# Optimization experiments

Measured on AMD Instinct MI355X. Metric: run time of the kernel, lower is better.

Reference implementation:

```python
import jax, jax.numpy as jnp
import numpy as np

NEG_SLOPE = 0.2  # LeakyReLU(0.2)


def setup_inputs() -> dict:
    key = jax.random.key(0)
    k0, k1, kw, kb = jax.random.split(key, 4)
    B, N, M, D, H = 1, 1024, 1024, 256, 128
    z0 = jax.random.normal(k0, (B, N, D), dtype=jnp.float32)
    z1 = jax.random.normal(k1, (B, M, D), dtype=jnp.float32)
    # Conv2d(D, H, 1) weight (H, D, 1, 1) squeezed to (H, D); bias (H,)
    W = jax.random.normal(kw, (H, D), dtype=jnp.float32) * (1.0 / np.sqrt(D))
    bias = jax.random.normal(kb, (H,), dtype=jnp.float32) * 0.01
    return {"z0": z0, "z1": z1, "W": W, "bias": bias}


def reference(z0, z1, W, bias):
    # torch: z_mul[b,d,n,m] = z0[b,n,d] * z1[b,m,d]; c = conv1x1(z_mul); LeakyReLU
    # Fused: 1x1 conv over channel D is a contraction -> single einsum, no (b,D,N,M) intermediate.
    c = jnp.einsum('bnd,bmd,hd->bhnm', z0, z1, W) + bias[None, :, None, None]
    return jnp.where(c >= 0, c, NEG_SLOPE * c)
```

## Files before the change

### kernel.cpp

```cpp
#include <hip/hip_runtime.h>
#include <cstdint>

#define AS1 __attribute__((address_space(1)))
#define AS3 __attribute__((address_space(3)))

typedef __bf16 v8bf __attribute__((ext_vector_type(8)));
typedef float  v4f  __attribute__((ext_vector_type(4)));

__device__ __forceinline__ uint32_t f2u(float f) {
    union { float f; uint32_t u; } v; v.f = f; return v.u;
}
__device__ __forceinline__ uint16_t f2bf_rne(float f) {
    uint32_t u = f2u(f);
    return (uint16_t)((u + 0x7FFFu + ((u >> 16) & 1u)) >> 16);
}
__device__ __forceinline__ uint32_t pack2(float a, float b) {
    return (uint32_t)f2bf_rne(a) | ((uint32_t)f2bf_rne(b) << 16);
}
__device__ __forceinline__ void async16(const void* g, void* l) {
    __builtin_amdgcn_global_load_lds((AS1 const void*)g, (AS3 void*)l, 16, 0, 0);
}

__global__ __launch_bounds__(256)
void prep_kernel(const float* __restrict__ z0, const float* __restrict__ z1,
                 const float* __restrict__ W,
                 uint16_t* __restrict__ Aall, uint16_t* __restrict__ Bbf)
{
    const int b = blockIdx.x;
    if (b < 16384) {
        const size_t e0 = ((size_t)b * 256 + threadIdx.x) * 8;
        const int h  = (int)(e0 >> 18);
        const int nd = (int)(e0 & 0x3FFFFu);
        const int d0 = (int)(e0 & 255u);
        float4 za = *(const float4*)(z0 + nd);
        float4 zb = *(const float4*)(z0 + nd + 4);
        float4 wa = *(const float4*)(W + h * 256 + d0);
        float4 wb = *(const float4*)(W + h * 256 + d0 + 4);
        uint4 r;
        r.x = pack2(za.x * wa.x, za.y * wa.y);
        r.y = pack2(za.z * wa.z, za.w * wa.w);
        r.z = pack2(zb.x * wb.x, zb.y * wb.y);
        r.w = pack2(zb.z * wb.z, zb.w * wb.w);
        *(uint4*)(Aall + e0) = r;
    } else {
        const size_t e0 = ((size_t)(b - 16384) * 256 + threadIdx.x) * 8;
        float4 za = *(const float4*)(z1 + e0);
        float4 zb = *(const float4*)(z1 + e0 + 4);
        uint4 r;
        r.x = pack2(za.x, za.y);
        r.y = pack2(za.z, za.w);
        r.z = pack2(zb.x, zb.y);
        r.w = pack2(zb.z, zb.w);
        *(uint4*)(Bbf + e0) = r;
    }
}

__global__ __launch_bounds__(256)
void gemm_kernel(const uint16_t* __restrict__ Aall, const uint16_t* __restrict__ Bbf,
                 const float* __restrict__ bias, float* __restrict__ out)
{
    __shared__ __align__(16) uint16_t aT[2][128 * 64];
    __shared__ __align__(16) uint16_t bT[2][128 * 64];

    const int t = threadIdx.x, wave = t >> 6, lane = t & 63;

    const int wg   = blockIdx.x;
    const int work = ((wg & 7) << 10) | (wg >> 3);
    const int h    = work >> 6;
    const int n0   = ((work >> 3) & 7) << 7;
    const int m0   = (work & 7) << 7;

    const uint16_t* Ab = Aall + ((size_t)h << 18) + ((size_t)n0 << 8);
    const uint16_t* Bb = Bbf + ((size_t)m0 << 8);

    const int srow = lane >> 3;
    const int slot = lane & 7;
    const int swz8 = (slot ^ srow) << 3;

    v4f acc[4][4];
#pragma unroll
    for (int r = 0; r < 4; ++r)
#pragma unroll
        for (int c = 0; c < 4; ++c) acc[r][c] = (v4f){0.f, 0.f, 0.f, 0.f};

    const int mbw = (wave & 1) * 64;
    const int nb  = (wave >> 1) * 64;
    const int fr  = lane & 15;
    const int q   = lane >> 4;
    const int sx  = fr & 7;

#pragma unroll
    for (int j = 0; j < 4; ++j) {
        const int row = wave * 32 + j * 8;
        async16(Ab + (size_t)(row + srow) * 256 + swz8, &aT[0][row * 64]);
        async16(Bb + (size_t)(row + srow) * 256 + swz8, &bT[0][row * 64]);
    }
    __syncthreads();

#pragma unroll
    for (int ks = 0; ks < 4; ++ks) {
        const int cur = ks & 1, nxt = cur ^ 1;
        if (ks < 3) {
            const int kel = (ks + 1) * 64 + swz8;
#pragma unroll
            for (int j = 0; j < 4; ++j) {
                const int row = wave * 32 + j * 8;
                async16(Ab + (size_t)(row + srow) * 256 + kel, &aT[nxt][row * 64]);
                async16(Bb + (size_t)(row + srow) * 256 + kel, &bT[nxt][row * 64]);
            }
        }
#pragma unroll
        for (int ksl = 0; ksl < 2; ++ksl) {
            const int ko = ((((ksl << 2) | q) ^ sx) << 3);
            v8bf am[4], bn[4];
#pragma unroll
            for (int r = 0; r < 4; ++r)
                am[r] = *(const v8bf*)&bT[cur][(mbw + r * 16 + fr) * 64 + ko];
#pragma unroll
            for (int c = 0; c < 4; ++c)
                bn[c] = *(const v8bf*)&aT[cur][(nb + c * 16 + fr) * 64 + ko];
#pragma unroll
            for (int r = 0; r < 4; ++r)
#pragma unroll
                for (int c = 0; c < 4; ++c)
                    acc[r][c] = __builtin_amdgcn_mfma_f32_16x16x32_bf16(am[r], bn[c], acc[r][c], 0, 0, 0);
        }
        __syncthreads();
    }

    const float bsf = bias[h];
    float* outB = out + ((size_t)h << 20) + ((size_t)n0 << 10) + m0;
    const int mq = (lane >> 4) * 4;
#pragma unroll
    for (int r = 0; r < 4; ++r) {
#pragma unroll
        for (int c = 0; c < 4; ++c) {
            const int n = nb + c * 16 + fr;
            const int m = mbw + r * 16 + mq;
            float4 o;
            float v0 = acc[r][c][0] + bsf; o.x = (v0 >= 0.f) ? v0 : 0.2f * v0;
            float v1 = acc[r][c][1] + bsf; o.y = (v1 >= 0.f) ? v1 : 0.2f * v1;
            float v2 = acc[r][c][2] + bsf; o.z = (v2 >= 0.f) ? v2 : 0.2f * v2;
            float v3 = acc[r][c][3] + bsf; o.w = (v3 >= 0.f) ? v3 : 0.2f * v3;
            *(float4*)(outB + ((size_t)n << 10) + m) = o;
        }
    }
}

__global__ __launch_bounds__(256)
void gemm_fb(const float* __restrict__ z0, const float* __restrict__ z1,
             const float* __restrict__ W, const float* __restrict__ bias,
             float* __restrict__ out)
{
    __shared__ __align__(16) uint16_t aT[128 * 32];
    __shared__ __align__(16) uint16_t bT[128 * 32];
    const int t = threadIdx.x, wave = t >> 6, lane = t & 63;
    const int h = blockIdx.z, n0 = blockIdx.y * 128, m0 = blockIdx.x * 128;
    const float* Ab = z0 + (size_t)n0 * 256;
    const float* Bb = z1 + (size_t)m0 * 256;
    const int rowA = t >> 2, col8 = (t & 3) * 8;

    v4f acc[4][4];
#pragma unroll
    for (int r = 0; r < 4; ++r)
#pragma unroll
        for (int c = 0; c < 4; ++c) acc[r][c] = (v4f){0.f, 0.f, 0.f, 0.f};

    const int mbw = (wave & 1) * 64, nb = (wave >> 1) * 64;
    const int fr = lane & 15, kq = (lane >> 4) * 8;

    for (int ks = 0; ks < 8; ++ks) {
        const int k0 = ks * 32;
        float4 wa = *(const float4*)(W + h * 256 + k0 + col8);
        float4 wb = *(const float4*)(W + h * 256 + k0 + col8 + 4);
#pragma unroll
        for (int i = 0; i < 2; ++i) {
            const int row = i * 64 + rowA;
            float4 za = *(const float4*)(Ab + (size_t)row * 256 + k0 + col8);
            float4 zb = *(const float4*)(Ab + (size_t)row * 256 + k0 + col8 + 4);
            uint4 r;
            r.x = pack2(za.x * wa.x, za.y * wa.y);
            r.y = pack2(za.z * wa.z, za.w * wa.w);
            r.z = pack2(zb.x * wb.x, zb.y * wb.y);
            r.w = pack2(zb.z * wb.z, zb.w * wb.w);
            *(uint4*)&aT[(i * 256 + t) * 8] = r;
            float4 ba = *(const float4*)(Bb + (size_t)row * 256 + k0 + col8);
            float4 bb = *(const float4*)(Bb + (size_t)row * 256 + k0 + col8 + 4);
            uint4 s;
            s.x = pack2(ba.x, ba.y);
            s.y = pack2(ba.z, ba.w);
            s.z = pack2(bb.x, bb.y);
            s.w = pack2(bb.z, bb.w);
            *(uint4*)&bT[(i * 256 + t) * 8] = s;
        }
        __syncthreads();

        v8bf am[4], bn[4];
#pragma unroll
        for (int r = 0; r < 4; ++r)
            am[r] = *(const v8bf*)&bT[(mbw + r * 16 + fr) * 32 + kq];
#pragma unroll
        for (int c = 0; c < 4; ++c)
            bn[c] = *(const v8bf*)&aT[(nb + c * 16 + fr) * 32 + kq];
#pragma unroll
        for (int r = 0; r < 4; ++r)
#pragma unroll
            for (int c = 0; c < 4; ++c)
                acc[r][c] = __builtin_amdgcn_mfma_f32_16x16x32_bf16(am[r], bn[c], acc[r][c], 0, 0, 0);
        __syncthreads();
    }

    const float bsf = bias[h];
    float* outB = out + ((size_t)h << 20) + ((size_t)n0 << 10) + m0;
    const int mq = (lane >> 4) * 4;
#pragma unroll
    for (int r = 0; r < 4; ++r) {
#pragma unroll
        for (int c = 0; c < 4; ++c) {
            const int n = nb + c * 16 + fr;
            const int m = mbw + r * 16 + mq;
            float4 o;
            float v0 = acc[r][c][0] + bsf; o.x = (v0 >= 0.f) ? v0 : 0.2f * v0;
            float v1 = acc[r][c][1] + bsf; o.y = (v1 >= 0.f) ? v1 : 0.2f * v1;
            float v2 = acc[r][c][2] + bsf; o.z = (v2 >= 0.f) ? v2 : 0.2f * v2;
            float v3 = acc[r][c][3] + bsf; o.w = (v3 >= 0.f) ? v3 : 0.2f * v3;
            *(float4*)(outB + ((size_t)n << 10) + m) = o;
        }
    }
}

extern "C" void kernel_launch(void* const* d_in, const int* in_sizes, int n_in,
                              void* d_out, int out_size, void* d_ws, size_t ws_size,
                              hipStream_t stream) {
    (void)in_sizes; (void)n_in; (void)out_size;
    const float* z0   = (const float*)d_in[0];
    const float* z1   = (const float*)d_in[1];
    const float* Wm   = (const float*)d_in[2];
    const float* bias = (const float*)d_in[3];
    float* out = (float*)d_out;

    const size_t aall_bytes = (size_t)128 * 1024 * 256 * 2;
    const size_t need = aall_bytes + (size_t)1024 * 256 * 2;
    if (ws_size >= need) {
        uint16_t* Aall = (uint16_t*)d_ws;
        uint16_t* Bbf  = (uint16_t*)((char*)d_ws + aall_bytes);
        prep_kernel<<<16512, 256, 0, stream>>>(z0, z1, Wm, Aall, Bbf);
        gemm_kernel<<<8192, 256, 0, stream>>>(Aall, Bbf, bias, out);
    } else {
        dim3 grid(8, 8, 128), block(256);
        gemm_fb<<<grid, block, 0, stream>>>(z0, z1, Wm, bias, out);
    }
}
```

Measured before the change: 666.5 us.

## Fuse W-scaling and bf16 conversion into GEMM, drop prep kernel and workspace

Replaces the two-kernel path (prep writing a per-head W-scaled bf16 copy of z0, then a GEMM reading it) with a single kernel. Each thread loads a row slice of fp32 z0 or z1 into registers, scales by W for the A side, converts to bf16 and stores swizzled into double-buffered LDS. Register prefetch of the next k-slice overlaps the MFMAs. This removes the large intermediate write/read and a launch, at the cost of more registers and per-block conversion ALU work.

```diff
diff --git a/kernel.cpp b/kernel.cpp
--- a/kernel.cpp
+++ b/kernel.cpp
@@ -1,63 +1,13 @@
 #include <hip/hip_runtime.h>
 #include <cstdint>
-
-#define AS1 __attribute__((address_space(1)))
-#define AS3 __attribute__((address_space(3)))
 
 typedef __bf16 v8bf __attribute__((ext_vector_type(8)));
 typedef float  v4f  __attribute__((ext_vector_type(4)));
 
-__device__ __forceinline__ uint32_t f2u(float f) {
-    union { float f; uint32_t u; } v; v.f = f; return v.u;
-}
-__device__ __forceinline__ uint16_t f2bf_rne(float f) {
-    uint32_t u = f2u(f);
-    return (uint16_t)((u + 0x7FFFu + ((u >> 16) & 1u)) >> 16);
-}
-__device__ __forceinline__ uint32_t pack2(float a, float b) {
-    return (uint32_t)f2bf_rne(a) | ((uint32_t)f2bf_rne(b) << 16);
-}
-__device__ __forceinline__ void async16(const void* g, void* l) {
-    __builtin_amdgcn_global_load_lds((AS1 const void*)g, (AS3 void*)l, 16, 0, 0);
-}
-
 __global__ __launch_bounds__(256)
-void prep_kernel(const float* __restrict__ z0, const float* __restrict__ z1,
-                 const float* __restrict__ W,
-                 uint16_t* __restrict__ Aall, uint16_t* __restrict__ Bbf)
-{
-    const int b = blockIdx.x;
-    if (b < 16384) {
-        const size_t e0 = ((size_t)b * 256 + threadIdx.x) * 8;
-        const int h  = (int)(e0 >> 18);
-        const int nd = (int)(e0 & 0x3FFFFu);
-        const int d0 = (int)(e0 & 255u);
-        float4 za = *(const float4*)(z0 + nd);
-        float4 zb = *(const float4*)(z0 + nd + 4);
-        float4 wa = *(const float4*)(W + h * 256 + d0);
-        float4 wb = *(const float4*)(W + h * 256 + d0 + 4);
-        uint4 r;
-        r.x = pack2(za.x * wa.x, za.y * wa.y);
-        r.y = pack2(za.z * wa.z, za.w * wa.w);
-        r.z = pack2(zb.x * wb.x, zb.y * wb.y);
-        r.w = pack2(zb.z * wb.z, zb.w * wb.w);
-        *(uint4*)(Aall + e0) = r;
-    } else {
-        const size_t e0 = ((size_t)(b - 16384) * 256 + threadIdx.x) * 8;
-        float4 za = *(const float4*)(z1 + e0);
-        float4 zb = *(const float4*)(z1 + e0 + 4);
-        uint4 r;
-        r.x = pack2(za.x, za.y);
-        r.y = pack2(za.z, za.w);
-        r.z = pack2(zb.x, zb.y);
-        r.w = pack2(zb.z, zb.w);
-        *(uint4*)(Bbf + e0) = r;
-    }
-}
-
-__global__ __launch_bounds__(256)
-void gemm_kernel(const uint16_t* __restrict__ Aall, const uint16_t* __restrict__ Bbf,
-                 const float* __restrict__ bias, float* __restrict__ out)
+void fused_gemm(const float* __restrict__ z0, const float* __restrict__ z1,
+                const float* __restrict__ W, const float* __restrict__ bias,
+                float* __restrict__ out)
 {
     __shared__ __align__(16) uint16_t aT[2][128 * 64];
     __shared__ __align__(16) uint16_t bT[2][128 * 64];
@@ -70,12 +20,32 @@
     const int n0   = ((work >> 3) & 7) << 7;
     const int m0   = (work & 7) << 7;
 
-    const uint16_t* Ab = Aall + ((size_t)h << 18) + ((size_t)n0 << 8);
-    const uint16_t* Bb = Bbf + ((size_t)m0 << 8);
+    const float* Wr = W + h * 256;
 
-    const int srow = lane >> 3;
-    const int slot = lane & 7;
-    const int swz8 = (slot ^ srow) << 3;
+    const bool isA = (t < 128);
+    const int  srow = t & 127;
+    const int  sx7  = srow & 7;
+    const float* src = (isA ? z0 + ((size_t)n0 << 8) : z1 + ((size_t)m0 << 8))
+                       + ((size_t)srow << 8);
+
+    float4 g[16];
+
+    auto convert_write = [&](uint16_t* dst, int k0) {
+#pragma unroll
+        for (int s = 0; s < 8; ++s) {
+            float4 u = g[2 * s], v = g[2 * s + 1];
+            if (isA) {
+                float4 wu = *(const float4*)(Wr + k0 + s * 8);
+                float4 wv = *(const float4*)(Wr + k0 + s * 8 + 4);
+                u.x *= wu.x; u.y *= wu.y; u.z *= wu.z; u.w *= wu.w;
+                v.x *= wv.x; v.y *= wv.y; v.z *= wv.z; v.w *= wv.w;
+            }
+            v8bf pk;
+            pk[0] = (__bf16)u.x; pk[1] = (__bf16)u.y; pk[2] = (__bf16)u.z; pk[3] = (__bf16)u.w;
+            pk[4] = (__bf16)v.x; pk[5] = (__bf16)v.y; pk[6] = (__bf16)v.z; pk[7] = (__bf16)v.w;
+            *(v8bf*)&dst[(srow << 6) + ((s ^ sx7) << 3)] = pk;
+        }
+    };
 
     v4f acc[4][4];
 #pragma unroll
@@ -90,25 +60,20 @@
     const int sx  = fr & 7;
 
 #pragma unroll
-    for (int j = 0; j < 4; ++j) {
-        const int row = wave * 32 + j * 8;
-        async16(Ab + (size_t)(row + srow) * 256 + swz8, &aT[0][row * 64]);
-        async16(Bb + (size_t)(row + srow) * 256 + swz8, &bT[0][row * 64]);
-    }
+    for (int i = 0; i < 16; ++i) g[i] = *(const float4*)(src + i * 4);
+    convert_write(isA ? aT[0] : bT[0], 0);
     __syncthreads();
 
 #pragma unroll
     for (int ks = 0; ks < 4; ++ks) {
         const int cur = ks & 1, nxt = cur ^ 1;
+
         if (ks < 3) {
-            const int kel = (ks + 1) * 64 + swz8;
+            const int k0n = (ks + 1) * 64;
 #pragma unroll
-            for (int j = 0; j < 4; ++j) {
-                const int row = wave * 32 + j * 8;
-                async16(Ab + (size_t)(row + srow) * 256 + kel, &aT[nxt][row * 64]);
-                async16(Bb + (size_t)(row + srow) * 256 + kel, &bT[nxt][row * 64]);
-            }
+            for (int i = 0; i < 16; ++i) g[i] = *(const float4*)(src + k0n + i * 4);
         }
+
 #pragma unroll
         for (int ksl = 0; ksl < 2; ++ksl) {
             const int ko = ((((ksl << 2) | q) ^ sx) << 3);
@@ -125,88 +90,10 @@
                 for (int c = 0; c < 4; ++c)
                     acc[r][c] = __builtin_amdgcn_mfma_f32_16x16x32_bf16(am[r], bn[c], acc[r][c], 0, 0, 0);
         }
-        __syncthreads();
-    }
 
-    const float bsf = bias[h];
-    float* outB = out + ((size_t)h << 20) + ((size_t)n0 << 10) + m0;
-    const int mq = (lane >> 4) * 4;
-#pragma unroll
-    for (int r = 0; r < 4; ++r) {
-#pragma unroll
-        for (int c = 0; c < 4; ++c) {
-            const int n = nb + c * 16 + fr;
-            const int m = mbw + r * 16 + mq;
-            float4 o;
-            float v0 = acc[r][c][0] + bsf; o.x = (v0 >= 0.f) ? v0 : 0.2f * v0;
-            float v1 = acc[r][c][1] + bsf; o.y = (v1 >= 0.f) ? v1 : 0.2f * v1;
-            float v2 = acc[r][c][2] + bsf; o.z = (v2 >= 0.f) ? v2 : 0.2f * v2;
-            float v3 = acc[r][c][3] + bsf; o.w = (v3 >= 0.f) ? v3 : 0.2f * v3;
-            *(float4*)(outB + ((size_t)n << 10) + m) = o;
-        }
-    }
-}
+        if (ks < 3)
+            convert_write(isA ? aT[nxt] : bT[nxt], (ks + 1) * 64);
 
-__global__ __launch_bounds__(256)
-void gemm_fb(const float* __restrict__ z0, const float* __restrict__ z1,
-             const float* __restrict__ W, const float* __restrict__ bias,
-             float* __restrict__ out)
-{
-    __shared__ __align__(16) uint16_t aT[128 * 32];
-    __shared__ __align__(16) uint16_t bT[128 * 32];
-    const int t = threadIdx.x, wave = t >> 6, lane = t & 63;
-    const int h = blockIdx.z, n0 = blockIdx.y * 128, m0 = blockIdx.x * 128;
-    const float* Ab = z0 + (size_t)n0 * 256;
-    const float* Bb = z1 + (size_t)m0 * 256;
-    const int rowA = t >> 2, col8 = (t & 3) * 8;
-
-    v4f acc[4][4];
-#pragma unroll
-    for (int r = 0; r < 4; ++r)
-#pragma unroll
-        for (int c = 0; c < 4; ++c) acc[r][c] = (v4f){0.f, 0.f, 0.f, 0.f};
-
-    const int mbw = (wave & 1) * 64, nb = (wave >> 1) * 64;
-    const int fr = lane & 15, kq = (lane >> 4) * 8;
-
-    for (int ks = 0; ks < 8; ++ks) {
-        const int k0 = ks * 32;
-        float4 wa = *(const float4*)(W + h * 256 + k0 + col8);
-        float4 wb = *(const float4*)(W + h * 256 + k0 + col8 + 4);
-#pragma unroll
-        for (int i = 0; i < 2; ++i) {
-            const int row = i * 64 + rowA;
-            float4 za = *(const float4*)(Ab + (size_t)row * 256 + k0 + col8);
-            float4 zb = *(const float4*)(Ab + (size_t)row * 256 + k0 + col8 + 4);
-            uint4 r;
-            r.x = pack2(za.x * wa.x, za.y * wa.y);
-            r.y = pack2(za.z * wa.z, za.w * wa.w);
-            r.z = pack2(zb.x * wb.x, zb.y * wb.y);
-            r.w = pack2(zb.z * wb.z, zb.w * wb.w);
-            *(uint4*)&aT[(i * 256 + t) * 8] = r;
-            float4 ba = *(const float4*)(Bb + (size_t)row * 256 + k0 + col8);
-            float4 bb = *(const float4*)(Bb + (size_t)row * 256 + k0 + col8 + 4);
-            uint4 s;
-            s.x = pack2(ba.x, ba.y);
-            s.y = pack2(ba.z, ba.w);
-            s.z = pack2(bb.x, bb.y);
-            s.w = pack2(bb.z, bb.w);
-            *(uint4*)&bT[(i * 256 + t) * 8] = s;
-        }
-        __syncthreads();
-
-        v8bf am[4], bn[4];
-#pragma unroll
-        for (int r = 0; r < 4; ++r)
-            am[r] = *(const v8bf*)&bT[(mbw + r * 16 + fr) * 32 + kq];
-#pragma unroll
-        for (int c = 0; c < 4; ++c)
-            bn[c] = *(const v8bf*)&aT[(nb + c * 16 + fr) * 32 + kq];
-#pragma unroll
-        for (int r = 0; r < 4; ++r)
-#pragma unroll
-            for (int c = 0; c < 4; ++c)
-                acc[r][c] = __builtin_amdgcn_mfma_f32_16x16x32_bf16(am[r], bn[c], acc[r][c], 0, 0, 0);
         __syncthreads();
     }
 
@@ -232,22 +119,12 @@
 extern "C" void kernel_launch(void* const* d_in, const int* in_sizes, int n_in,
                               void* d_out, int out_size, void* d_ws, size_t ws_size,
                               hipStream_t stream) {
-    (void)in_sizes; (void)n_in; (void)out_size;
+    (void)in_sizes; (void)n_in; (void)out_size; (void)d_ws; (void)ws_size;
     const float* z0   = (const float*)d_in[0];
     const float* z1   = (const float*)d_in[1];
     const float* Wm   = (const float*)d_in[2];
     const float* bias = (const float*)d_in[3];
     float* out = (float*)d_out;
 
-    const size_t aall_bytes = (size_t)128 * 1024 * 256 * 2;
-    const size_t need = aall_bytes + (size_t)1024 * 256 * 2;
-    if (ws_size >= need) {
-        uint16_t* Aall = (uint16_t*)d_ws;
-        uint16_t* Bbf  = (uint16_t*)((char*)d_ws + aall_bytes);
-        prep_kernel<<<16512, 256, 0, stream>>>(z0, z1, Wm, Aall, Bbf);
-        gemm_kernel<<<8192, 256, 0, stream>>>(Aall, Bbf, bias, out);
-    } else {
-        dim3 grid(8, 8, 128), block(256);
-        gemm_fb<<<grid, block, 0, stream>>>(z0, z1, Wm, bias, out);
-    }
+    fused_gemm<<<8192, 256, 0, stream>>>(z0, z1, Wm, bias, out);
 }
```

Result: slower. 724.4 us (+8.7%).
